# Kernel optimization log

Hardware: AMD Instinct MI355X
Metric: run time of the kernel (lower is better)

The kernel has to match this reference:

```python
import jax, jax.numpy as jnp
import numpy as np

B, IN_DIM, FEAT_DIM, MEM_SIZE, HID, OUT_DIM = 2048, 2048, 256, 100000, 2048, 1024


def setup_inputs() -> dict:
    key = jax.random.key(0)
    ks = jax.random.split(key, 14)
    w = lambda k, shape: (jax.random.normal(k, shape, jnp.float32) * 0.02)
    return {
        "x": jax.random.normal(ks[0], (B, IN_DIM), jnp.float32),
        # feature extractor: IN_DIM -> 512 -> 256 -> FEAT_DIM
        "W1": w(ks[1], (IN_DIM, 512)), "b1": jnp.zeros((512,), jnp.float32),
        "W2": w(ks[2], (512, 256)),    "b2": jnp.zeros((256,), jnp.float32),
        "W3": w(ks[3], (256, FEAT_DIM)), "b3": jnp.zeros((FEAT_DIM,), jnp.float32),
        # external memory table
        "memory": jax.random.normal(ks[4], (MEM_SIZE, FEAT_DIM), jnp.float32),
        # task column: 2*FEAT_DIM -> HID -> HID -> OUT_DIM
        "Wt1": w(ks[5], (2 * FEAT_DIM, HID)), "bt1": jnp.zeros((HID,), jnp.float32),
        "Wt2": w(ks[6], (HID, HID)),          "bt2": jnp.zeros((HID,), jnp.float32),
        "Wo": w(ks[7], (HID, OUT_DIM)),       "bo": jnp.zeros((OUT_DIM,), jnp.float32),
    }


def reference(x, W1, b1, W2, b2, W3, b3, memory, Wt1, bt1, Wt2, bt2, Wo, bo):
    # ---- feature extractor MLP ----
    f = jax.nn.relu(x @ W1 + b1)
    f = jax.nn.relu(f @ W2 + b2)
    f = f @ W3 + b3                      # [B, FEAT_DIM]

    # ---- ExternalMemory.query ----
    # torch code detaches both features and memory before scoring (CPU/numba)
    fd = jax.lax.stop_gradient(f)
    md = jax.lax.stop_gradient(memory)
    bsz = f.shape[0]
    # scores[i] = -sum_{b,d} (f_bd - m_id)^2
    #           = -(B*||m_i||^2 - 2 m_i . sum_b f_b + sum||f||^2)
    f_sum = jnp.sum(fd, axis=0)                         # [D]
    f_sq = jnp.sum(fd * fd)                             # scalar
    m_sq = jnp.sum(md * md, axis=1)                     # [M]
    scores = -(bsz * m_sq - 2.0 * (md @ f_sum) + f_sq)  # [M]

    k = min(MEM_SIZE, bsz)  # == B here (required for the concat below)
    _, idx = jax.lax.top_k(scores, k)                   # descending, like torch.topk
    mem_out = memory[idx]                               # [B, FEAT_DIM] (grad flows to memory)

    # ---- concat + task column ----
    h = jnp.concatenate([f, mem_out], axis=-1)          # [B, 2*FEAT_DIM]
    h = jax.nn.relu(h @ Wt1 + bt1)
    h = jax.nn.relu(h @ Wt2 + bt2)
    return h @ Wo + bo                                  # [B, OUT_DIM]
```

## Files before the change

kernel.cpp:

```cpp
#include <hip/hip_runtime.h>

typedef unsigned int u32;
typedef unsigned long long u64;
typedef unsigned short u16;

typedef __attribute__((ext_vector_type(8))) short bf16x8;
typedef __attribute__((ext_vector_type(4))) float f32x4;

#define FEAT 256
#define MEMN 100000

#define OPAQ(x) asm volatile("" : "+v"(x))

static __device__ __forceinline__ u16 f2bf(float x){
  u32 u = __float_as_uint(x);
  u32 r = u + 0x7fffu + ((u >> 16) & 1u);
  return (u16)(r >> 16);
}

template<int RELU>
__global__ __launch_bounds__(256) void gemm_seq_k(const float* __restrict__ A,
                                                  const float* __restrict__ Bm,
                                                  const float* __restrict__ bias,
                                                  float* __restrict__ C,
                                                  int M, int N, int K){
  __shared__ float As[64][33];
  __shared__ float Bs[32][65];
  const int t = threadIdx.x;
  const int tx = t & 15, ty = t >> 4;
  const int bm = blockIdx.y << 6, bn = blockIdx.x << 6;
  float acc[4][4], mast[4][4];
  #pragma unroll
  for (int i = 0; i < 4; i++)
    #pragma unroll
    for (int j = 0; j < 4; j++){ acc[i][j] = 0.f; mast[i][j] = 0.f; }
  for (int kt = 0; kt < K; kt += 32){
    #pragma unroll
    for (int i = 0; i < 8; i++){
      int o = t + (i << 8);
      int r = o >> 5, c = o & 31;
      As[r][c] = A[(u64)(bm + r) * K + kt + c];
    }
    #pragma unroll
    for (int i = 0; i < 8; i++){
      int o = t + (i << 8);
      int r = o >> 6, c = o & 63;
      Bs[r][c] = Bm[(u64)(kt + r) * N + bn + c];
    }
    __syncthreads();
    #pragma unroll
    for (int k = 0; k < 32; k++){
      float a[4], b[4];
      #pragma unroll
      for (int i = 0; i < 4; i++) a[i] = As[(ty << 2) + i][k];
      #pragma unroll
      for (int j = 0; j < 4; j++) b[j] = Bs[k][(tx << 2) + j];
      #pragma unroll
      for (int i = 0; i < 4; i++)
        #pragma unroll
        for (int j = 0; j < 4; j++) acc[i][j] = fmaf(a[i], b[j], acc[i][j]);
    }
    __syncthreads();
    if (((kt + 32) % 384) == 0 || (kt + 32) == K){
      #pragma unroll
      for (int i = 0; i < 4; i++)
        #pragma unroll
        for (int j = 0; j < 4; j++){ mast[i][j] = mast[i][j] + acc[i][j]; acc[i][j] = 0.f; }
    }
  }
  #pragma unroll
  for (int i = 0; i < 4; i++){
    int row = bm + (ty << 2) + i;
    #pragma unroll
    for (int j = 0; j < 4; j++){
      int col = bn + (tx << 2) + j;
      float v = mast[i][j] + bias[col];
      if (RELU) v = v > 0.f ? v : 0.f;
      C[(u64)row * N + col] = v;
    }
  }
}

__global__ __launch_bounds__(256) void fsum_seq_k(const float* __restrict__ f,
                                                  float* __restrict__ fsum){
  int d = threadIdx.x;
  float s = 0.f;
  for (int r = 0; r < 2048; r++) s += f[(u64)r * FEAT + d];
  fsum[d] = s;
}

__device__ __forceinline__ float block128_sq_avx512(const float4* base, int off, int swz){
  float e0[16], e1[16], f0[16], s16[16];
  #pragma unroll
  for (int j = 0; j < 8; j++){
    #pragma unroll
    for (int q = 0; q < 4; q++){
      float4 v = base[off + (((j << 2) + q) ^ swz)];
      float p0 = v.x * v.x, p1 = v.y * v.y, p2 = v.z * v.z, p3 = v.w * v.w;
      OPAQ(p0); OPAQ(p1); OPAQ(p2); OPAQ(p3);
      int l = q << 2;
      if (j == 0 || j == 4){ e0[l] = p0; e0[l+1] = p1; e0[l+2] = p2; e0[l+3] = p3; }
      else if (j == 1 || j == 5){ e0[l] += p0; e0[l+1] += p1; e0[l+2] += p2; e0[l+3] += p3; }
      else if (j == 2 || j == 6){ e1[l] = p0; e1[l+1] = p1; e1[l+2] = p2; e1[l+3] = p3; }
      else { e1[l] += p0; e1[l+1] += p1; e1[l+2] += p2; e1[l+3] += p3; }
    }
    if (j == 3){
      #pragma unroll
      for (int l = 0; l < 16; l++) f0[l] = e0[l] + e1[l];
    }
    if (j == 7){
      #pragma unroll
      for (int l = 0; l < 16; l++) s16[l] = f0[l] + (e0[l] + e1[l]);
    }
  }
  float h8[8], h4[4], h2[2];
  #pragma unroll
  for (int l = 0; l < 8; l++) h8[l] = s16[l] + s16[l + 8];
  #pragma unroll
  for (int l = 0; l < 4; l++) h4[l] = h8[l] + h8[l + 4];
  h2[0] = h4[0] + h4[2]; h2[1] = h4[1] + h4[3];
  return h2[0] + h2[1];
}

__global__ __launch_bounds__(256) void leaf_k(const float* __restrict__ f,
                                              float* __restrict__ lf){
  int b = blockIdx.x * 256 + threadIdx.x;
  lf[b] = block128_sq_avx512((const float4*)(f + (u64)b * 128), 0, 0);
}

__global__ __launch_bounds__(1024) void tree_k(const float* __restrict__ lf,
                                               float* __restrict__ fsq){
  __shared__ float sa[4096];
  __shared__ float sb[2048];
  int t = threadIdx.x;
  for (int i = t; i < 4096; i += 1024) sa[i] = lf[i];
  __syncthreads();
  float* src = sa; float* dst = sb;
  for (int len = 2048; len >= 1; len >>= 1){
    for (int i = t; i < len; i += 1024) dst[i] = src[2 * i] + src[2 * i + 1];
    __syncthreads();
    float* tmp = src; src = dst; dst = tmp;
  }
  if (t == 0) *fsq = src[0];
}

__global__ __launch_bounds__(256) void score_row_k(const float* __restrict__ mem,
                                                   const float* __restrict__ fsum,
                                                   const float* __restrict__ fsq_p,
                                                   u32* __restrict__ keys,
                                                   u32* __restrict__ hist,
                                                   u32* __restrict__ hist2){
  __shared__ __align__(16) float fs[256];
  __shared__ float4 buf[2][64][64];
  __shared__ u32 lh2[256];
  const int t = threadIdx.x;
  fs[t] = fsum[t];
  lh2[t] = 0;
  const int base = blockIdx.x * 256;
  const int w = t >> 6;
  const float4* mg = (const float4*)mem;
  const float4* s4 = (const float4*)fs;

  for (int p = 0; p < 4; p++){
    #pragma unroll
    for (int i = 0; i < 16; i++){
      int g = (i << 8) + t;
      int lr = g >> 6, q = g & 63;
      int gr = base + (p << 6) + lr;
      if (gr < MEMN) buf[p & 1][lr][q ^ (lr & 7)] = mg[(u64)gr * 64 + q];
    }
    __syncthreads();
    if (w == p){
      int row = base + t;
      if (row < MEMN){
        const int lane = t & 63;
        const float4* rowp = &buf[p & 1][lane][0];
        const int swz = lane & 7;
        float dpr[8];
        #pragma unroll
        for (int j = 0; j < 8; j++) dpr[j] = 0.f;
        #pragma unroll
        for (int kb = 0; kb < 64; kb++){
          float4 mv = rowp[kb ^ swz];
          float4 fv = s4[kb];
          int j0 = (kb & 1) ? 4 : 0;
          dpr[j0 + 0] = fmaf(mv.x, fv.x, dpr[j0 + 0]);
          dpr[j0 + 1] = fmaf(mv.y, fv.y, dpr[j0 + 1]);
          dpr[j0 + 2] = fmaf(mv.z, fv.z, dpr[j0 + 2]);
          dpr[j0 + 3] = fmaf(mv.w, fv.w, dpr[j0 + 3]);
        }
        float r0 = block128_sq_avx512(rowp, 0, swz);
        float r1 = block128_sq_avx512(rowp, 32, swz);
        float msq = r0 + r1;
        float b0 = dpr[0] + dpr[4], b1 = dpr[1] + dpr[5];
        float b2 = dpr[2] + dpr[6], b3 = dpr[3] + dpr[7];
        float dp = (b0 + b1) + (b2 + b3);
        float t1 = 2048.0f * msq;
        float t2 = 2.0f * dp;
        float d3 = t1 - t2;  OPAQ(d3);
        float d4 = d3 + fsq_p[0];
        float s = -d4;
        u32 bb = __float_as_uint(s);
        u32 key = (bb & 0x80000000u) ? ~bb : (bb | 0x80000000u);
        keys[row] = key;
        atomicAdd(&hist[key >> 14], 1u);
        atomicAdd(&lh2[key >> 24], 1u);
      }
    }
  }
  __syncthreads();
  u32 v = lh2[t];
  if (v) atomicAdd(&hist2[t], v);
}

__global__ __launch_bounds__(1024) void find_T_k(const u32* __restrict__ hist,
                                                 const u32* __restrict__ hist2,
                                                 u32* __restrict__ Tbin){
  __shared__ u32 h2[256];
  __shared__ int sh_c;
  __shared__ u32 sh_run;
  __shared__ u32 sa[1024], sb[1024];
  int t = threadIdx.x;
  if (t < 256) h2[t] = hist2[t];
  __syncthreads();
  if (t == 0){
    u32 run = 0; int cstar = 0;
    for (int c = 255; c >= 0; c--){
      u32 v = h2[c];
      if (run + v >= 2048u){ cstar = c; break; }
      run += v;
    }
    sh_c = cstar; sh_run = run;
  }
  __syncthreads();
  int cstar = sh_c; u32 run = sh_run;
  sa[t] = hist[cstar * 1024 + t];
  __syncthreads();
  u32* src = sa; u32* dst = sb;
  for (int off = 1; off < 1024; off <<= 1){
    u32 v = src[t];
    if (t + off < 1024) v += src[t + off];
    dst[t] = v;
    __syncthreads();
    u32* tmp = src; src = dst; dst = tmp;
  }
  u32 suf  = src[t];
  u32 sufn = (t < 1023) ? src[t + 1] : 0u;
  if (run + suf >= 2048u && !(run + sufn >= 2048u)) *Tbin = (u32)(cstar * 1024 + t);
}

__global__ __launch_bounds__(256) void compact_k(const u32* __restrict__ keys,
                                                 const u32* __restrict__ Tbin,
                                                 u64* __restrict__ pk,
                                                 u32* __restrict__ counter){
  int i = blockIdx.x * 256 + threadIdx.x;
  if (i >= MEMN) return;
  u32 k = keys[i];
  if ((k >> 14) >= *Tbin){
    u32 p = atomicAdd(counter, 1u);
    if (p < 4096u) pk[p] = ((u64)k << 32) | (u32)(0xFFFFFFFFu - (u32)i);
  }
}

__global__ __launch_bounds__(1024) void sort_k(const u64* __restrict__ pkin,
                                               u32* __restrict__ idxo){
  __shared__ u64 k[4096];
  for (int i = threadIdx.x; i < 4096; i += 1024) k[i] = pkin[i];
  __syncthreads();
  for (int size = 2; size <= 4096; size <<= 1){
    for (int stride = size >> 1; stride; stride >>= 1){
      #pragma unroll 2
      for (int pp = 0; pp < 2; pp++){
        int p = threadIdx.x + pp * 1024;
        int i = ((p / stride) * (stride << 1)) + (p % stride);
        int j = i + stride;
        u64 a = k[i], b = k[j];
        bool desc_ok = (a >= b);
        bool up = ((i & size) == 0);
        if (up ? !desc_ok : desc_ok){ k[i] = b; k[j] = a; }
      }
      __syncthreads();
    }
  }
  for (int i = threadIdx.x; i < 2048; i += 1024) idxo[i] = 0xFFFFFFFFu - (u32)k[i];
}

__global__ __launch_bounds__(256) void build_h_k(const float* __restrict__ f,
                                                 const float* __restrict__ mem,
                                                 const u32* __restrict__ idx,
                                                 u16* __restrict__ h){
  int r = blockIdx.x, t = threadIdx.x;
  h[(u64)r * 512 + t] = f2bf(f[(u64)r * FEAT + t]);
  h[(u64)r * 512 + 256 + t] = f2bf(mem[(u64)idx[r] * FEAT + t]);
}

__global__ void convT_k(const float* __restrict__ W, u16* __restrict__ WT, int K, int N){
  __shared__ float tile[32][33];
  int tx = threadIdx.x, ty = threadIdx.y;
  int bk = blockIdx.y << 5, bn = blockIdx.x << 5;
  #pragma unroll
  for (int i = 0; i < 4; i++){
    int r = ty + (i << 3);
    tile[r][tx] = W[(u64)(bk + r) * N + bn + tx];
  }
  __syncthreads();
  #pragma unroll
  for (int i = 0; i < 4; i++){
    int n = ty + (i << 3);
    WT[(u64)(bn + n) * K + bk + tx] = f2bf(tile[tx][n]);
  }
}

static __device__ __forceinline__ void gl_lds16(const u16* g, u16* l){
  __builtin_amdgcn_global_load_lds((const __attribute__((address_space(1))) void*)g,
                                   (__attribute__((address_space(3))) void*)l, 16, 0, 0);
}

template<int RELU, int OUTBF>
__global__ __launch_bounds__(256) void gemm_bf16_k(const u16* __restrict__ A,
                                                   const u16* __restrict__ BT,
                                                   const float* __restrict__ bias,
                                                   void* __restrict__ Cout,
                                                   int M, int N, int K){
  __shared__ u16 As[128 * 32];
  __shared__ u16 Bs[128 * 32];
  const int t = threadIdx.x;
  const int w = t >> 6, lane = t & 63;
  const int bm = blockIdx.y << 7, bn = blockIdx.x << 7;
  f32x4 acc[4][4];
  #pragma unroll
  for (int i = 0; i < 4; i++)
    #pragma unroll
    for (int j = 0; j < 4; j++) acc[i][j] = (f32x4){0.f, 0.f, 0.f, 0.f};
  const int row0 = (w >> 1) << 6, col0 = (w & 1) << 6;
  for (int kt = 0; kt < K; kt += 32){
    #pragma unroll
    for (int j = 0; j < 2; j++){
      int e = (((j << 2) + w) << 9) + (lane << 3);
      int r = e >> 5, c = e & 31;
      gl_lds16(A  + (u64)(bm + r) * K + kt + c, As + (((j << 2) + w) << 9));
      gl_lds16(BT + (u64)(bn + r) * K + kt + c, Bs + (((j << 2) + w) << 9));
    }
    __syncthreads();
    bf16x8 af[4], bfr[4];
    #pragma unroll
    for (int i = 0; i < 4; i++){
      af[i]  = *(const bf16x8*)(As + (row0 + (i << 4) + (lane & 15)) * 32 + ((lane >> 4) << 3));
      bfr[i] = *(const bf16x8*)(Bs + (col0 + (i << 4) + (lane & 15)) * 32 + ((lane >> 4) << 3));
    }
    #pragma unroll
    for (int i = 0; i < 4; i++)
      #pragma unroll
      for (int j = 0; j < 4; j++)
        acc[i][j] = __builtin_amdgcn_mfma_f32_16x16x32_bf16(af[i], bfr[j], acc[i][j], 0, 0, 0);
    __syncthreads();
  }
  #pragma unroll
  for (int i = 0; i < 4; i++){
    #pragma unroll
    for (int j = 0; j < 4; j++){
      #pragma unroll
      for (int r = 0; r < 4; r++){
        int row = bm + row0 + (i << 4) + ((lane >> 4) << 2) + r;
        int col = bn + col0 + (j << 4) + (lane & 15);
        float v = acc[i][j][r] + bias[col];
        if (RELU) v = v > 0.f ? v : 0.f;
        if (OUTBF) ((u16*)Cout)[(u64)row * N + col] = f2bf(v);
        else       ((float*)Cout)[(u64)row * N + col] = v;
      }
    }
  }
}

extern "C" void kernel_launch(void* const* d_in, const int* in_sizes, int n_in,
                              void* d_out, int out_size, void* d_ws, size_t ws_size,
                              hipStream_t stream){
  const float* x   = (const float*)d_in[0];
  const float* W1  = (const float*)d_in[1];
  const float* b1  = (const float*)d_in[2];
  const float* W2  = (const float*)d_in[3];
  const float* b2  = (const float*)d_in[4];
  const float* W3  = (const float*)d_in[5];
  const float* b3  = (const float*)d_in[6];
  const float* mem = (const float*)d_in[7];
  const float* Wt1 = (const float*)d_in[8];
  const float* bt1 = (const float*)d_in[9];
  const float* Wt2 = (const float*)d_in[10];
  const float* bt2 = (const float*)d_in[11];
  const float* Wo  = (const float*)d_in[12];
  const float* bo  = (const float*)d_in[13];

  char* ws = (char*)d_ws;
  float* f1   = (float*)(ws + 0);
  u32*   keys = (u32*)  (ws + 0);
  u32*   hist = (u32*)  (ws + 0x080000);
  u32*   hist2= (u32*)  (ws + 0x180000);
  u32*   Tbin = (u32*)  (ws + 0x180000 + 1024);
  u32*   cnt  = (u32*)  (ws + 0x180000 + 1028);
  u64*   pk   = (u64*)  (ws + 0x180000 + 4096);
  u32*   idxo = (u32*)  (ws + 0x180000 + 40960);
  float* fsum = (float*)(ws + 0x180000 + 49152);
  float* lf   = (float*)(ws + 0x180000 + 50176);
  float* fsq  = (float*)(ws + 0x180000 + 66560);
  float* f2   = (float*)(ws + (4ull  << 20));
  float* f    = (float*)(ws + (6ull  << 20));
  u16*   h    = (u16*)  (ws + (8ull  << 20));
  u16*   W1T  = (u16*)  (ws + (10ull << 20));
  u16*   W2T  = (u16*)  (ws + (12ull << 20));
  u16*   WoT  = (u16*)  (ws + (20ull << 20));
  u16*   T1   = (u16*)  (ws + (24ull << 20));
  u16*   T2   = (u16*)  (ws + (32ull << 20));

  dim3 blk(256);
  gemm_seq_k<1><<<dim3(8, 32),  blk, 0, stream>>>(x,  W1, b1, f1, 2048, 512, 2048);
  gemm_seq_k<1><<<dim3(4, 32),  blk, 0, stream>>>(f1, W2, b2, f2, 2048, 256, 512);
  gemm_seq_k<0><<<dim3(4, 32),  blk, 0, stream>>>(f2, W3, b3, f,  2048, 256, 256);
  hipMemsetAsync(hist, 0, 1048576, stream);
  hipMemsetAsync(ws + 0x180000, 0, 36864, stream);
  fsum_seq_k <<<dim3(1),   blk,        0, stream>>>(f, fsum);
  leaf_k     <<<dim3(16),  blk,        0, stream>>>(f, lf);
  tree_k     <<<dim3(1),   dim3(1024), 0, stream>>>(lf, fsq);
  score_row_k<<<dim3(391), blk,        0, stream>>>(mem, fsum, fsq, keys, hist, hist2);
  find_T_k   <<<dim3(1),   dim3(1024), 0, stream>>>(hist, hist2, Tbin);
  compact_k  <<<dim3(391), blk,        0, stream>>>(keys, Tbin, pk, cnt);
  sort_k     <<<dim3(1),   dim3(1024), 0, stream>>>(pk, idxo);
  build_h_k<<<dim3(2048), blk, 0, stream>>>(f, mem, idxo, h);
  convT_k<<<dim3(64, 16), dim3(32, 8), 0, stream>>>(Wt1, W1T, 512,  2048);
  convT_k<<<dim3(64, 64), dim3(32, 8), 0, stream>>>(Wt2, W2T, 2048, 2048);
  convT_k<<<dim3(32, 64), dim3(32, 8), 0, stream>>>(Wo,  WoT, 2048, 1024);
  gemm_bf16_k<1, 1><<<dim3(16, 16), blk, 0, stream>>>(h,  W1T, bt1, T1, 2048, 2048, 512);
  gemm_bf16_k<1, 1><<<dim3(16, 16), blk, 0, stream>>>(T1, W2T, bt2, T2, 2048, 2048, 2048);
  gemm_bf16_k<0, 0><<<dim3(8, 16),  blk, 0, stream>>>(T2, WoT, bo, (float*)d_out, 2048, 1024, 2048);
}
```

Before: 545.4 us.

## Double-buffer FP32 feature GEMM and split scoring into 64-row blocks

The FP32 feature-extractor GEMM now uses 512 threads, stores A transposed in double-buffered shared memory and prefetches the next K tile into registers while computing the current one. This removes one barrier per tile and allows vectorised float4/float2 LDS reads. The memory-scoring kernel moves from 256-thread blocks, where only one wave computed per phase, to 64-thread blocks each handling 64 rows. That gives 1563 blocks with all lanes active and less idle waiting. Each thread now holds fewer accumulators, so reuse per thread drops, and the change adds more blocks and more hist2 atomics.

After: 505.9 us. 7.2% less time.

```diff
diff --git a/kernel.cpp b/kernel.cpp
--- a/kernel.cpp
+++ b/kernel.cpp
@@ -19,61 +19,80 @@
 }
 
 template<int RELU>
-__global__ __launch_bounds__(256) void gemm_seq_k(const float* __restrict__ A,
+__global__ __launch_bounds__(512) void gemm_seq_k(const float* __restrict__ A,
                                                   const float* __restrict__ Bm,
                                                   const float* __restrict__ bias,
                                                   float* __restrict__ C,
                                                   int M, int N, int K){
-  __shared__ float As[64][33];
-  __shared__ float Bs[32][65];
+  __shared__ float At[2][32][68];
+  __shared__ float Bs[2][32][68];
   const int t = threadIdx.x;
-  const int tx = t & 15, ty = t >> 4;
+  const int tx = t & 31, ty = t >> 5;
   const int bm = blockIdx.y << 6, bn = blockIdx.x << 6;
-  float acc[4][4], mast[4][4];
+  float acc[4][2], mast[4][2];
   #pragma unroll
   for (int i = 0; i < 4; i++)
     #pragma unroll
-    for (int j = 0; j < 4; j++){ acc[i][j] = 0.f; mast[i][j] = 0.f; }
+    for (int j = 0; j < 2; j++){ acc[i][j] = 0.f; mast[i][j] = 0.f; }
+
+  float pa[4], pb[4];
+  #pragma unroll
+  for (int i = 0; i < 4; i++){
+    int o = t + (i << 9);
+    pa[i] = A [(u64)(bm + (o >> 5)) * K + (o & 31)];
+    pb[i] = Bm[(u64)((o >> 6)) * N + bn + (o & 63)];
+  }
+  #pragma unroll
+  for (int i = 0; i < 4; i++){
+    int o = t + (i << 9);
+    At[0][o & 31][o >> 5] = pa[i];
+    Bs[0][o >> 6][o & 63] = pb[i];
+  }
+  __syncthreads();
+
+  int cur = 0;
   for (int kt = 0; kt < K; kt += 32){
-    #pragma unroll
-    for (int i = 0; i < 8; i++){
-      int o = t + (i << 8);
-      int r = o >> 5, c = o & 31;
-      As[r][c] = A[(u64)(bm + r) * K + kt + c];
-    }
-    #pragma unroll
-    for (int i = 0; i < 8; i++){
-      int o = t + (i << 8);
-      int r = o >> 6, c = o & 63;
-      Bs[r][c] = Bm[(u64)(kt + r) * N + bn + c];
-    }
-    __syncthreads();
+    const int nxt = kt + 32;
+    if (nxt < K){
+      #pragma unroll
+      for (int i = 0; i < 4; i++){
+        int o = t + (i << 9);
+        pa[i] = A [(u64)(bm + (o >> 5)) * K + nxt + (o & 31)];
+        pb[i] = Bm[(u64)(nxt + (o >> 6)) * N + bn + (o & 63)];
+      }
+    }
     #pragma unroll
     for (int k = 0; k < 32; k++){
-      float a[4], b[4];
-      #pragma unroll
-      for (int i = 0; i < 4; i++) a[i] = As[(ty << 2) + i][k];
-      #pragma unroll
-      for (int j = 0; j < 4; j++) b[j] = Bs[k][(tx << 2) + j];
+      float4 av = *reinterpret_cast<const float4*>(&At[cur][k][ty << 2]);
+      float2 bv = *reinterpret_cast<const float2*>(&Bs[cur][k][tx << 1]);
+      acc[0][0] = fmaf(av.x, bv.x, acc[0][0]); acc[0][1] = fmaf(av.x, bv.y, acc[0][1]);
+      acc[1][0] = fmaf(av.y, bv.x, acc[1][0]); acc[1][1] = fmaf(av.y, bv.y, acc[1][1]);
+      acc[2][0] = fmaf(av.z, bv.x, acc[2][0]); acc[2][1] = fmaf(av.z, bv.y, acc[2][1]);
+      acc[3][0] = fmaf(av.w, bv.x, acc[3][0]); acc[3][1] = fmaf(av.w, bv.y, acc[3][1]);
+    }
+    if ((nxt % 384) == 0 || nxt == K){
       #pragma unroll
       for (int i = 0; i < 4; i++)
         #pragma unroll
-        for (int j = 0; j < 4; j++) acc[i][j] = fmaf(a[i], b[j], acc[i][j]);
-    }
-    __syncthreads();
-    if (((kt + 32) % 384) == 0 || (kt + 32) == K){
-      #pragma unroll
-      for (int i = 0; i < 4; i++)
-        #pragma unroll
-        for (int j = 0; j < 4; j++){ mast[i][j] = mast[i][j] + acc[i][j]; acc[i][j] = 0.f; }
+        for (int j = 0; j < 2; j++){ mast[i][j] = mast[i][j] + acc[i][j]; acc[i][j] = 0.f; }
+    }
+    if (nxt < K){
+      #pragma unroll
+      for (int i = 0; i < 4; i++){
+        int o = t + (i << 9);
+        At[cur ^ 1][o & 31][o >> 5] = pa[i];
+        Bs[cur ^ 1][o >> 6][o & 63] = pb[i];
+      }
+      __syncthreads();
+      cur ^= 1;
     }
   }
   #pragma unroll
   for (int i = 0; i < 4; i++){
     int row = bm + (ty << 2) + i;
     #pragma unroll
-    for (int j = 0; j < 4; j++){
-      int col = bn + (tx << 2) + j;
+    for (int j = 0; j < 2; j++){
+      int col = bn + (tx << 1) + j;
       float v = mast[i][j] + bias[col];
       if (RELU) v = v > 0.f ? v : 0.f;
       C[(u64)row * N + col] = v;
@@ -144,73 +163,68 @@
   if (t == 0) *fsq = src[0];
 }
 
-__global__ __launch_bounds__(256) void score_row_k(const float* __restrict__ mem,
-                                                   const float* __restrict__ fsum,
-                                                   const float* __restrict__ fsq_p,
-                                                   u32* __restrict__ keys,
-                                                   u32* __restrict__ hist,
-                                                   u32* __restrict__ hist2){
+__global__ __launch_bounds__(64) void score_row_k(const float* __restrict__ mem,
+                                                  const float* __restrict__ fsum,
+                                                  const float* __restrict__ fsq_p,
+                                                  u32* __restrict__ keys,
+                                                  u32* __restrict__ hist,
+                                                  u32* __restrict__ hist2){
   __shared__ __align__(16) float fs[256];
-  __shared__ float4 buf[2][64][64];
+  __shared__ float4 buf[64][64];
   __shared__ u32 lh2[256];
   const int t = threadIdx.x;
-  fs[t] = fsum[t];
-  lh2[t] = 0;
-  const int base = blockIdx.x * 256;
-  const int w = t >> 6;
+  #pragma unroll
+  for (int i = 0; i < 4; i++){ fs[t + (i << 6)] = fsum[t + (i << 6)]; lh2[t + (i << 6)] = 0; }
+  const int base = blockIdx.x << 6;
   const float4* mg = (const float4*)mem;
   const float4* s4 = (const float4*)fs;
 
-  for (int p = 0; p < 4; p++){
-    #pragma unroll
-    for (int i = 0; i < 16; i++){
-      int g = (i << 8) + t;
-      int lr = g >> 6, q = g & 63;
-      int gr = base + (p << 6) + lr;
-      if (gr < MEMN) buf[p & 1][lr][q ^ (lr & 7)] = mg[(u64)gr * 64 + q];
-    }
-    __syncthreads();
-    if (w == p){
-      int row = base + t;
-      if (row < MEMN){
-        const int lane = t & 63;
-        const float4* rowp = &buf[p & 1][lane][0];
-        const int swz = lane & 7;
-        float dpr[8];
-        #pragma unroll
-        for (int j = 0; j < 8; j++) dpr[j] = 0.f;
-        #pragma unroll
-        for (int kb = 0; kb < 64; kb++){
-          float4 mv = rowp[kb ^ swz];
-          float4 fv = s4[kb];
-          int j0 = (kb & 1) ? 4 : 0;
-          dpr[j0 + 0] = fmaf(mv.x, fv.x, dpr[j0 + 0]);
-          dpr[j0 + 1] = fmaf(mv.y, fv.y, dpr[j0 + 1]);
-          dpr[j0 + 2] = fmaf(mv.z, fv.z, dpr[j0 + 2]);
-          dpr[j0 + 3] = fmaf(mv.w, fv.w, dpr[j0 + 3]);
-        }
-        float r0 = block128_sq_avx512(rowp, 0, swz);
-        float r1 = block128_sq_avx512(rowp, 32, swz);
-        float msq = r0 + r1;
-        float b0 = dpr[0] + dpr[4], b1 = dpr[1] + dpr[5];
-        float b2 = dpr[2] + dpr[6], b3 = dpr[3] + dpr[7];
-        float dp = (b0 + b1) + (b2 + b3);
-        float t1 = 2048.0f * msq;
-        float t2 = 2.0f * dp;
-        float d3 = t1 - t2;  OPAQ(d3);
-        float d4 = d3 + fsq_p[0];
-        float s = -d4;
-        u32 bb = __float_as_uint(s);
-        u32 key = (bb & 0x80000000u) ? ~bb : (bb | 0x80000000u);
-        keys[row] = key;
-        atomicAdd(&hist[key >> 14], 1u);
-        atomicAdd(&lh2[key >> 24], 1u);
-      }
-    }
-  }
-  __syncthreads();
-  u32 v = lh2[t];
-  if (v) atomicAdd(&hist2[t], v);
+  #pragma unroll 8
+  for (int i = 0; i < 64; i++){
+    int gr = base + i;
+    if (gr < MEMN) buf[i][t ^ (i & 7)] = mg[(u64)gr * 64 + t];
+  }
+  __syncthreads();
+  int row = base + t;
+  if (row < MEMN){
+    const float4* rowp = &buf[t][0];
+    const int swz = t & 7;
+    float dpr[8];
+    #pragma unroll
+    for (int j = 0; j < 8; j++) dpr[j] = 0.f;
+    #pragma unroll
+    for (int kb = 0; kb < 64; kb++){
+      float4 mv = rowp[kb ^ swz];
+      float4 fv = s4[kb];
+      int j0 = (kb & 1) ? 4 : 0;
+      dpr[j0 + 0] = fmaf(mv.x, fv.x, dpr[j0 + 0]);
+      dpr[j0 + 1] = fmaf(mv.y, fv.y, dpr[j0 + 1]);
+      dpr[j0 + 2] = fmaf(mv.z, fv.z, dpr[j0 + 2]);
+      dpr[j0 + 3] = fmaf(mv.w, fv.w, dpr[j0 + 3]);
+    }
+    float r0 = block128_sq_avx512(rowp, 0, swz);
+    float r1 = block128_sq_avx512(rowp, 32, swz);
+    float msq = r0 + r1;
+    float b0 = dpr[0] + dpr[4], b1 = dpr[1] + dpr[5];
+    float b2 = dpr[2] + dpr[6], b3 = dpr[3] + dpr[7];
+    float dp = (b0 + b1) + (b2 + b3);
+    float t1 = 2048.0f * msq;
+    float t2 = 2.0f * dp;
+    float d3 = t1 - t2;  OPAQ(d3);
+    float d4 = d3 + fsq_p[0];
+    float s = -d4;
+    u32 bb = __float_as_uint(s);
+    u32 key = (bb & 0x80000000u) ? ~bb : (bb | 0x80000000u);
+    keys[row] = key;
+    atomicAdd(&hist[key >> 14], 1u);
+    atomicAdd(&lh2[key >> 24], 1u);
+  }
+  __syncthreads();
+  #pragma unroll
+  for (int i = 0; i < 4; i++){
+    u32 v = lh2[t + (i << 6)];
+    if (v) atomicAdd(&hist2[t + (i << 6)], v);
+  }
 }
 
 __global__ __launch_bounds__(1024) void find_T_k(const u32* __restrict__ hist,
@@ -411,19 +425,19 @@
   u16*   T1   = (u16*)  (ws + (24ull << 20));
   u16*   T2   = (u16*)  (ws + (32ull << 20));
 
-  dim3 blk(256);
-  gemm_seq_k<1><<<dim3(8, 32),  blk, 0, stream>>>(x,  W1, b1, f1, 2048, 512, 2048);
-  gemm_seq_k<1><<<dim3(4, 32),  blk, 0, stream>>>(f1, W2, b2, f2, 2048, 256, 512);
-  gemm_seq_k<0><<<dim3(4, 32),  blk, 0, stream>>>(f2, W3, b3, f,  2048, 256, 256);
+  dim3 blk(256), blk512(512);
+  gemm_seq_k<1><<<dim3(8, 32),  blk512, 0, stream>>>(x,  W1, b1, f1, 2048, 512, 2048);
+  gemm_seq_k<1><<<dim3(4, 32),  blk512, 0, stream>>>(f1, W2, b2, f2, 2048, 256, 512);
+  gemm_seq_k<0><<<dim3(4, 32),  blk512, 0, stream>>>(f2, W3, b3, f,  2048, 256, 256);
   hipMemsetAsync(hist, 0, 1048576, stream);
   hipMemsetAsync(ws + 0x180000, 0, 36864, stream);
-  fsum_seq_k <<<dim3(1),   blk,        0, stream>>>(f, fsum);
-  leaf_k     <<<dim3(16),  blk,        0, stream>>>(f, lf);
-  tree_k     <<<dim3(1),   dim3(1024), 0, stream>>>(lf, fsq);
-  score_row_k<<<dim3(391), blk,        0, stream>>>(mem, fsum, fsq, keys, hist, hist2);
-  find_T_k   <<<dim3(1),   dim3(1024), 0, stream>>>(hist, hist2, Tbin);
-  compact_k  <<<dim3(391), blk,        0, stream>>>(keys, Tbin, pk, cnt);
-  sort_k     <<<dim3(1),   dim3(1024), 0, stream>>>(pk, idxo);
+  fsum_seq_k <<<dim3(1),    blk,        0, stream>>>(f, fsum);
+  leaf_k     <<<dim3(16),   blk,        0, stream>>>(f, lf);
+  tree_k     <<<dim3(1),    dim3(1024), 0, stream>>>(lf, fsq);
+  score_row_k<<<dim3(1563), dim3(64),   0, stream>>>(mem, fsum, fsq, keys, hist, hist2);
+  find_T_k   <<<dim3(1),    dim3(1024), 0, stream>>>(hist, hist2, Tbin);
+  compact_k  <<<dim3(391),  blk,        0, stream>>>(keys, Tbin, pk, cnt);
+  sort_k     <<<dim3(1),    dim3(1024), 0, stream>>>(pk, idxo);
   build_h_k<<<dim3(2048), blk, 0, stream>>>(f, mem, idxo, h);
   convT_k<<<dim3(64, 16), dim3(32, 8), 0, stream>>>(Wt1, W1T, 512,  2048);
   convT_k<<<dim3(64, 64), dim3(32, 8), 0, stream>>>(Wt2, W2T, 2048, 2048);
```
